# Optimization experiments

Measured on AMD Instinct MI355X. Metric: run time of the kernel, lower is better.

Reference implementation:

```python
import jax, jax.numpy as jnp
import numpy as np

B, S, DIM, H = 4, 2048, 1024, 16
DEPTH = DIM // H


def setup_inputs() -> dict:
    key = jax.random.key(0)
    ks = jax.random.split(key, 12)
    s = 0.02
    return {
        "Q": jax.random.normal(ks[0], (B, S, DIM), jnp.float32),
        "K": jax.random.normal(ks[1], (B, S, DIM), jnp.float32),
        "V": jax.random.normal(ks[2], (B, S, DIM), jnp.float32),
        "mask": jax.random.randint(ks[3], (B, 1, 1, S), 0, 2).astype(jnp.float32),
        "Wq": jax.random.normal(ks[4], (DIM, DIM), jnp.float32) * s,
        "bq": jnp.zeros((DIM,), jnp.float32),
        "Wk": jax.random.normal(ks[5], (DIM, DIM), jnp.float32) * s,
        "bk": jnp.zeros((DIM,), jnp.float32),
        "Wv": jax.random.normal(ks[6], (DIM, DIM), jnp.float32) * s,
        "bv": jnp.zeros((DIM,), jnp.float32),
        "Wo": jax.random.normal(ks[7], (DIM, DIM), jnp.float32) * s,
        "bo": jnp.zeros((DIM,), jnp.float32),
    }


def _split_heads(x):
    # [B,S,DIM] -> [B,H,S,DEPTH]
    return x.reshape(x.shape[0], x.shape[1], H, DEPTH).transpose(0, 2, 1, 3)


def reference(Q, K, V, mask, Wq, bq, Wk, bk, Wv, bv, Wo, bo):
    q = _split_heads(Q @ Wq + bq)
    k = _split_heads(K @ Wk + bk)
    v = _split_heads(V @ Wv + bv)
    # scaled dot-product attention; note original scales by sqrt(depth) = last dim of K after split
    logits = jnp.einsum("bhqd,bhkd->bhqk", q, k) / jnp.sqrt(jnp.float32(DEPTH))
    logits = logits + mask * -1e9
    attn = jax.nn.softmax(logits, axis=-1)
    ctx = jnp.einsum("bhqk,bhkd->bhqd", attn, v)
    ctx = ctx.transpose(0, 2, 1, 3).reshape(Q.shape[0], Q.shape[1], DIM)
    return ctx @ Wo + bo
```

## Files before the change

kernel.cpp:

```cpp
#include <hip/hip_runtime.h>

typedef short s16x8 __attribute__((ext_vector_type(8)));
typedef short s16x4 __attribute__((ext_vector_type(4)));
typedef float f32x4 __attribute__((ext_vector_type(4)));

#define MFMA32(a, b, c) __builtin_amdgcn_mfma_f32_16x16x32_bf16((a), (b), (c), 0, 0, 0)

#if defined(__HIP_DEVICE_COMPILE__)
#define MFMA16(a, b, c) __builtin_amdgcn_mfma_f32_16x16x16bf16_1k((a), (b), (c), 0, 0, 0)
#else
#define MFMA16(a, b, c) (c)
#endif

__device__ __forceinline__ void stage16(const unsigned short* g, unsigned short* l) {
#if defined(__HIP_DEVICE_COMPILE__)
  __builtin_amdgcn_global_load_lds((const __attribute__((address_space(1))) unsigned int*)g,
                                   (__attribute__((address_space(3))) unsigned int*)l, 16, 0, 0);
#endif
}

__device__ __forceinline__ unsigned short f2b(float f) {
  unsigned int u = __builtin_bit_cast(unsigned int, f);
  unsigned int r = u + 0x7FFFu + ((u >> 16) & 1u);
  return (unsigned short)(r >> 16);
}
__device__ __forceinline__ unsigned int pk2(float a, float b) {
  return (unsigned int)f2b(a) | ((unsigned int)f2b(b) << 16);
}
__device__ __forceinline__ s16x4 mk4(float p0, float p1, float p2, float p3) {
  uint2 u;
  u.x = pk2(p0, p1);
  u.y = pk2(p2, p3);
  return __builtin_bit_cast(s16x4, u);
}
__device__ __forceinline__ float fast_exp2(float x) {
#if defined(__HIP_DEVICE_COMPILE__) && __has_builtin(__builtin_amdgcn_exp2f)
  return __builtin_amdgcn_exp2f(x);
#else
  return exp2f(x);
#endif
}

__global__ __launch_bounds__(256) void castq(const float* __restrict__ X,
                                             unsigned short* __restrict__ Y) {
  int i = blockIdx.x * 256 + threadIdx.x;
  float4 f0 = ((const float4*)X)[i * 2];
  float4 f1 = ((const float4*)X)[i * 2 + 1];
  uint4 u;
  u.x = pk2(f0.x, f0.y);
  u.y = pk2(f0.z, f0.w);
  u.z = pk2(f1.x, f1.y);
  u.w = pk2(f1.z, f1.w);
  ((uint4*)Y)[i] = u;
}

__global__ void wtrans(const float* __restrict__ W0, const float* __restrict__ W1,
                       const float* __restrict__ W2, const float* __restrict__ W3,
                       unsigned short* __restrict__ T0, unsigned short* __restrict__ T1,
                       unsigned short* __restrict__ T2, unsigned short* __restrict__ T3) {
  const float* W;
  unsigned short* T;
  switch (blockIdx.z) {
    case 0: W = W0; T = T0; break;
    case 1: W = W1; T = T1; break;
    case 2: W = W2; T = T2; break;
    default: W = W3; T = T3; break;
  }
  __shared__ float tile[32][33];
  const int n0 = blockIdx.x << 5;
  const int k0 = blockIdx.y << 5;
  const int tx = threadIdx.x;
  const int ty = threadIdx.y;
#pragma unroll
  for (int j = 0; j < 4; ++j)
    tile[ty + 8 * j][tx] = W[(size_t)(k0 + ty + 8 * j) * 1024 + n0 + tx];
  __syncthreads();
#pragma unroll
  for (int j = 0; j < 4; ++j)
    T[(size_t)(n0 + ty + 8 * j) * 1024 + k0 + tx] = f2b(tile[tx][ty + 8 * j]);
}

template <int MODE>
__global__ __launch_bounds__(256, 2) void gemm_bt(const unsigned short* __restrict__ A,
                                                  const unsigned short* __restrict__ Bt,
                                                  const float* __restrict__ bias,
                                                  void* __restrict__ Cout, float oscale) {
  __shared__ __align__(16) unsigned short As[128 * 32];
  __shared__ __align__(16) unsigned short Bs[128 * 32];
  const int n0 = blockIdx.x * 128;
  const int m0 = blockIdx.y * 128;
  const int tid = threadIdx.x;
  const int w = tid >> 6;
  const int lane = tid & 63;
  const int lr = lane & 15;
  const int lg = lane >> 4;
  const int wm = (w >> 1) << 6;
  const int wn = (w & 1) << 6;

  const int srow = w * 16 + (lane >> 2);
  const int sseg = lane & 3;
  const unsigned short* Ag0 = A + (size_t)(m0 + srow) * 1024 + sseg * 8;
  const unsigned short* Ag1 = A + (size_t)(m0 + 64 + srow) * 1024 + sseg * 8;
  const unsigned short* Bg0 = Bt + (size_t)(n0 + srow) * 1024 + sseg * 8;
  const unsigned short* Bg1 = Bt + (size_t)(n0 + 64 + srow) * 1024 + sseg * 8;
  unsigned short* Al0 = &As[(w * 16) * 32];
  unsigned short* Al1 = &As[(64 + w * 16) * 32];
  unsigned short* Bl0 = &Bs[(w * 16) * 32];
  unsigned short* Bl1 = &Bs[(64 + w * 16) * 32];

  f32x4 acc[4][4];
#pragma unroll
  for (int i = 0; i < 4; ++i)
#pragma unroll
    for (int j = 0; j < 4; ++j) {
      f32x4 z = {0.f, 0.f, 0.f, 0.f};
      acc[i][j] = z;
    }

  for (int k0 = 0; k0 < 1024; k0 += 32) {
    stage16(Ag0 + k0, Al0);
    stage16(Ag1 + k0, Al1);
    stage16(Bg0 + k0, Bl0);
    stage16(Bg1 + k0, Bl1);
    __syncthreads();
    s16x8 af[4], bfr[4];
#pragma unroll
    for (int mt = 0; mt < 4; ++mt) af[mt] = *(const s16x8*)&As[(wm + mt * 16 + lr) * 32 + lg * 8];
#pragma unroll
    for (int nt = 0; nt < 4; ++nt) bfr[nt] = *(const s16x8*)&Bs[(wn + nt * 16 + lr) * 32 + lg * 8];
#pragma unroll
    for (int mt = 0; mt < 4; ++mt)
#pragma unroll
      for (int nt = 0; nt < 4; ++nt)
        acc[mt][nt] = MFMA32(af[mt], bfr[nt], acc[mt][nt]);
    __syncthreads();
  }

  float bcol[4];
#pragma unroll
  for (int nt = 0; nt < 4; ++nt) bcol[nt] = bias[n0 + wn + nt * 16 + lr];

#pragma unroll
  for (int mt = 0; mt < 4; ++mt)
#pragma unroll
    for (int nt = 0; nt < 4; ++nt)
#pragma unroll
      for (int r = 0; r < 4; ++r) {
        float v = (acc[mt][nt][r] + bcol[nt]) * oscale;
        int row = m0 + wm + mt * 16 + lg * 4 + r;
        int col = n0 + wn + nt * 16 + lr;
        if constexpr (MODE == 0) {
          int b = row >> 11, s = row & 2047, hh = col >> 6, d = col & 63;
          ((unsigned short*)Cout)[(((size_t)(b * 16 + hh) * 2048 + s) << 6) + d] = f2b(v);
        } else if constexpr (MODE == 1) {
          int b = row >> 11, s = row & 2047, hh = col >> 6, d = col & 63;
          ((unsigned short*)Cout)[(((size_t)(b * 16 + hh) * 64 + d) << 11) + s] = f2b(v);
        } else {
          ((float*)Cout)[(size_t)row * 1024 + col] = v;
        }
      }
}

__global__ __launch_bounds__(256, 4) void flash_attn(const unsigned short* __restrict__ qh,
                                                     const unsigned short* __restrict__ kh,
                                                     const unsigned short* __restrict__ vt,
                                                     const float* __restrict__ mask,
                                                     unsigned short* __restrict__ ctx) {
  const float c2 = 1.4426950408889634e9f;
  const int id = blockIdx.x;
  const int bh = id & 63;
  const int qtile = id >> 6;
  const int b = bh >> 4;
  const int h = bh & 15;
  const int q0 = qtile << 7;
  const int tid = threadIdx.x;
  const int w = tid >> 6;
  const int lane = tid & 63;
  const int lr = lane & 15;
  const int lg = lane >> 4;

  __shared__ __align__(16) unsigned short Ks[64 * 64];
  __shared__ __align__(16) unsigned short Vs[64 * 64];

  const unsigned short* qbase = qh + ((size_t)bh * 2048 + q0 + w * 32) * 64;
  const unsigned short* kbase = kh + (size_t)bh * 2048 * 64;
  const unsigned short* vbase = vt + (size_t)bh * 64 * 2048;
  const float* mbase = mask + b * 2048;

  const int rowc = lane >> 3;
  const int gseg = (lane & 7) ^ rowc;
  const unsigned short* kg0 = kbase + (size_t)(w * 16 + rowc) * 64 + gseg * 8;
  const unsigned short* kg1 = kbase + (size_t)(w * 16 + 8 + rowc) * 64 + gseg * 8;
  const unsigned short* vg0 = vbase + (size_t)(w * 16 + rowc) * 2048 + gseg * 8;
  const unsigned short* vg1 = vbase + (size_t)(w * 16 + 8 + rowc) * 2048 + gseg * 8;
  unsigned short* kl0 = &Ks[(w * 16 + 0) * 64];
  unsigned short* kl1 = &Ks[(w * 16 + 8) * 64];
  unsigned short* vl0 = &Vs[(w * 16 + 0) * 64];
  unsigned short* vl1 = &Vs[(w * 16 + 8) * 64];

  s16x8 qf[2][2];
#pragma unroll
  for (int qt = 0; qt < 2; ++qt)
#pragma unroll
    for (int kk = 0; kk < 2; ++kk)
      qf[qt][kk] = *(const s16x8*)(qbase + (qt * 16 + lr) * 64 + kk * 32 + lg * 8);

  const s16x4 ones = {(short)0x3F80, (short)0x3F80, (short)0x3F80, (short)0x3F80};

  f32x4 o_acc[2][4];
  f32x4 l_acc[2];
#pragma unroll
  for (int qt = 0; qt < 2; ++qt) {
    f32x4 z = {0.f, 0.f, 0.f, 0.f};
    l_acc[qt] = z;
#pragma unroll
    for (int dt = 0; dt < 4; ++dt) o_acc[qt][dt] = z;
  }

  for (int t0 = 0; t0 < 2048; t0 += 64) {
    stage16(kg0 + (size_t)t0 * 64, kl0);
    stage16(kg1 + (size_t)t0 * 64, kl1);
    stage16(vg0 + t0, vl0);
    stage16(vg1 + t0, vl1);
    float4 mk[4];
#pragma unroll
    for (int kt = 0; kt < 4; ++kt) mk[kt] = *(const float4*)(mbase + t0 + kt * 16 + lg * 4);
    __syncthreads();

    s16x4 pf[4][2];
    const int sw = lr & 7;
#pragma unroll
    for (int kt = 0; kt < 4; ++kt) {
      const int krow = kt * 16 + lr;
      s16x8 kf0 = *(const s16x8*)&Ks[krow * 64 + ((lg ^ sw) * 8)];
      s16x8 kf1 = *(const s16x8*)&Ks[krow * 64 + (((4 + lg) ^ sw) * 8)];
      float ml0 = mk[kt].x * c2, ml1 = mk[kt].y * c2;
      float ml2 = mk[kt].z * c2, ml3 = mk[kt].w * c2;
#pragma unroll
      for (int qt = 0; qt < 2; ++qt) {
        f32x4 s = {0.f, 0.f, 0.f, 0.f};
        s = MFMA32(kf0, qf[qt][0], s);
        s = MFMA32(kf1, qf[qt][1], s);
        pf[kt][qt] = mk4(fast_exp2(s[0] - ml0), fast_exp2(s[1] - ml1),
                         fast_exp2(s[2] - ml2), fast_exp2(s[3] - ml3));
      }
    }

#pragma unroll
    for (int kt = 0; kt < 4; ++kt) {
#pragma unroll
      for (int qt = 0; qt < 2; ++qt) l_acc[qt] = MFMA16(ones, pf[kt][qt], l_acc[qt]);
      const int phys = (kt * 2 + (lg >> 1)) ^ sw;
#pragma unroll
      for (int dt = 0; dt < 4; ++dt) {
        const int d = dt * 16 + lr;
        s16x4 vf = *(const s16x4*)&Vs[d * 64 + phys * 8 + (lg & 1) * 4];
#pragma unroll
        for (int qt = 0; qt < 2; ++qt) o_acc[qt][dt] = MFMA16(vf, pf[kt][qt], o_acc[qt][dt]);
      }
    }
    __syncthreads();
  }

#pragma unroll
  for (int qt = 0; qt < 2; ++qt) {
    float inv = 1.0f / l_acc[qt][0];
    int q = q0 + w * 32 + qt * 16 + lr;
    unsigned short* cp = ctx + ((size_t)(b * 2048 + q) * 16 + h) * 64 + lg * 4;
#pragma unroll
    for (int dt = 0; dt < 4; ++dt) {
      f32x4 o = o_acc[qt][dt];
      uint2 u;
      u.x = pk2(o[0] * inv, o[1] * inv);
      u.y = pk2(o[2] * inv, o[3] * inv);
      *(uint2*)(cp + dt * 16) = u;
    }
  }
}

extern "C" void kernel_launch(void* const* d_in, const int* in_sizes, int n_in,
                              void* d_out, int out_size, void* d_ws, size_t ws_size,
                              hipStream_t stream) {
  (void)in_sizes; (void)n_in; (void)out_size; (void)ws_size;
  const float* Q = (const float*)d_in[0];
  const float* K = (const float*)d_in[1];
  const float* V = (const float*)d_in[2];
  const float* mask = (const float*)d_in[3];
  const float* Wq = (const float*)d_in[4];
  const float* bq = (const float*)d_in[5];
  const float* Wk = (const float*)d_in[6];
  const float* bk = (const float*)d_in[7];
  const float* Wv = (const float*)d_in[8];
  const float* bv = (const float*)d_in[9];
  const float* Wo = (const float*)d_in[10];
  const float* bo = (const float*)d_in[11];

  char* ws = (char*)d_ws;
  unsigned short* wqt = (unsigned short*)(ws + (size_t)0);
  unsigned short* wkt = (unsigned short*)(ws + ((size_t)2 << 20));
  unsigned short* wvt = (unsigned short*)(ws + ((size_t)4 << 20));
  unsigned short* wot = (unsigned short*)(ws + ((size_t)6 << 20));
  unsigned short* qhb = (unsigned short*)(ws + ((size_t)8 << 20));
  unsigned short* khb = (unsigned short*)(ws + ((size_t)24 << 20));
  unsigned short* vtb = (unsigned short*)(ws + ((size_t)40 << 20));
  unsigned short* tmp = (unsigned short*)(ws + ((size_t)56 << 20));
  unsigned short* ctx = tmp;

  wtrans<<<dim3(32, 32, 4), dim3(32, 8), 0, stream>>>(Wq, Wk, Wv, Wo, wqt, wkt, wvt, wot);

  const float qscale = 0.18033688011112042f;
  dim3 gg(8, 64), bb(256);
  const int castBlocks = (8192 * 1024) / (256 * 8);

  castq<<<castBlocks, 256, 0, stream>>>(Q, tmp);
  gemm_bt<0><<<gg, bb, 0, stream>>>(tmp, wqt, bq, qhb, qscale);
  castq<<<castBlocks, 256, 0, stream>>>(K, tmp);
  gemm_bt<0><<<gg, bb, 0, stream>>>(tmp, wkt, bk, khb, 1.0f);
  castq<<<castBlocks, 256, 0, stream>>>(V, tmp);
  gemm_bt<1><<<gg, bb, 0, stream>>>(tmp, wvt, bv, vtb, 1.0f);

  flash_attn<<<dim3(1024), dim3(256), 0, stream>>>(qhb, khb, vtb, mask, ctx);

  gemm_bt<2><<<gg, bb, 0, stream>>>(ctx, wot, bo, d_out, 1.0f);
}
```

Baseline: 384.4 us.

## Multi-buffer GEMM LDS staging with async prefetch and use hardware bf16 pack

Reworks the projection GEMM main loop to use a 4-slot LDS ring. Loads are issued two K-steps ahead and gated by a partial vmcnt wait plus one barrier per iteration, replacing two full syncthreads per step, so global-to-LDS loads overlap the MFMA work. The software bf16 round/pack in the attention kernel is also replaced with the packed hardware conversion builtin where available. The ring grows LDS use fourfold to 64KB per block, which may limit occupancy under launch_bounds(256,2). The hand-coded waitcnt encoding must match the number of outstanding loads.

```diff
diff --git a/kernel.cpp b/kernel.cpp
--- a/kernel.cpp
+++ b/kernel.cpp
@@ -27,10 +27,18 @@
 __device__ __forceinline__ unsigned int pk2(float a, float b) {
   return (unsigned int)f2b(a) | ((unsigned int)f2b(b) << 16);
 }
+__device__ __forceinline__ unsigned int pkbf(float a, float b) {
+#if __has_builtin(__builtin_amdgcn_cvt_pk_bf16_f32)
+  auto t = __builtin_amdgcn_cvt_pk_bf16_f32(a, b);
+  return __builtin_bit_cast(unsigned int, t);
+#else
+  return pk2(a, b);
+#endif
+}
 __device__ __forceinline__ s16x4 mk4(float p0, float p1, float p2, float p3) {
   uint2 u;
-  u.x = pk2(p0, p1);
-  u.y = pk2(p2, p3);
+  u.x = pkbf(p0, p1);
+  u.y = pkbf(p2, p3);
   return __builtin_bit_cast(s16x4, u);
 }
 __device__ __forceinline__ float fast_exp2(float x) {
@@ -85,8 +93,8 @@
                                                   const unsigned short* __restrict__ Bt,
                                                   const float* __restrict__ bias,
                                                   void* __restrict__ Cout, float oscale) {
-  __shared__ __align__(16) unsigned short As[128 * 32];
-  __shared__ __align__(16) unsigned short Bs[128 * 32];
+  __shared__ __align__(16) unsigned short As[4][128 * 32];
+  __shared__ __align__(16) unsigned short Bs[4][128 * 32];
   const int n0 = blockIdx.x * 128;
   const int m0 = blockIdx.y * 128;
   const int tid = threadIdx.x;
@@ -103,10 +111,8 @@
   const unsigned short* Ag1 = A + (size_t)(m0 + 64 + srow) * 1024 + sseg * 8;
   const unsigned short* Bg0 = Bt + (size_t)(n0 + srow) * 1024 + sseg * 8;
   const unsigned short* Bg1 = Bt + (size_t)(n0 + 64 + srow) * 1024 + sseg * 8;
-  unsigned short* Al0 = &As[(w * 16) * 32];
-  unsigned short* Al1 = &As[(64 + w * 16) * 32];
-  unsigned short* Bl0 = &Bs[(w * 16) * 32];
-  unsigned short* Bl1 = &Bs[(64 + w * 16) * 32];
+  const int l0 = (w * 16) * 32;
+  const int l1 = (64 + w * 16) * 32;
 
   f32x4 acc[4][4];
 #pragma unroll
@@ -117,24 +123,47 @@
       acc[i][j] = z;
     }
 
-  for (int k0 = 0; k0 < 1024; k0 += 32) {
-    stage16(Ag0 + k0, Al0);
-    stage16(Ag1 + k0, Al1);
-    stage16(Bg0 + k0, Bl0);
-    stage16(Bg1 + k0, Bl1);
-    __syncthreads();
+  auto issue = [&](int i) {
+    const int k0 = i * 32;
+    const int s = i & 3;
+    stage16(Ag0 + k0, &As[s][l0]);
+    stage16(Ag1 + k0, &As[s][l1]);
+    stage16(Bg0 + k0, &Bs[s][l0]);
+    stage16(Bg1 + k0, &Bs[s][l1]);
+  };
+
+  auto body = [&](int i, bool last) {
+    asm volatile("" ::: "memory");
+#if defined(__HIP_DEVICE_COMPILE__)
+    if (last)
+      __builtin_amdgcn_s_waitcnt(0x0F70);
+    else
+      __builtin_amdgcn_s_waitcnt(0x0F74);
+    __builtin_amdgcn_s_barrier();
+#else
+    (void)last;
+#endif
+    asm volatile("" ::: "memory");
+    if (!last && i + 2 < 32) issue(i + 2);
+    const int s = i & 3;
     s16x8 af[4], bfr[4];
 #pragma unroll
-    for (int mt = 0; mt < 4; ++mt) af[mt] = *(const s16x8*)&As[(wm + mt * 16 + lr) * 32 + lg * 8];
-#pragma unroll
-    for (int nt = 0; nt < 4; ++nt) bfr[nt] = *(const s16x8*)&Bs[(wn + nt * 16 + lr) * 32 + lg * 8];
+    for (int mt = 0; mt < 4; ++mt)
+      af[mt] = *(const s16x8*)&As[s][(wm + mt * 16 + lr) * 32 + lg * 8];
+#pragma unroll
+    for (int nt = 0; nt < 4; ++nt)
+      bfr[nt] = *(const s16x8*)&Bs[s][(wn + nt * 16 + lr) * 32 + lg * 8];
 #pragma unroll
     for (int mt = 0; mt < 4; ++mt)
 #pragma unroll
       for (int nt = 0; nt < 4; ++nt)
         acc[mt][nt] = MFMA32(af[mt], bfr[nt], acc[mt][nt]);
-    __syncthreads();
-  }
+  };
+
+  issue(0);
+  issue(1);
+  for (int i = 0; i < 31; ++i) body(i, false);
+  body(31, true);
 
   float bcol[4];
 #pragma unroll
@@ -271,8 +300,8 @@
     for (int dt = 0; dt < 4; ++dt) {
       f32x4 o = o_acc[qt][dt];
       uint2 u;
-      u.x = pk2(o[0] * inv, o[1] * inv);
-      u.y = pk2(o[2] * inv, o[3] * inv);
+      u.x = pkbf(o[0] * inv, o[1] * inv);
+      u.y = pkbf(o[2] * inv, o[3] * inv);
       *(uint2*)(cp + dt * 16) = u;
     }
   }
```

Measured after the change: 406.2 us. 5.7% more time.
